# Kernel tuning notes

Measured on AMD Instinct MI355X. Metric: run time of the kernel, lower is better.

## Reference

```python
import jax, jax.numpy as jnp
import numpy as np

D_MODEL = 4096
D_HIDDEN = 32768
BATCH = 2048
K = 128
N_DEAD = 2048


def _ln(x, eps=1e-5):
    # torch .std() is unbiased (ddof=1)
    mu = jnp.mean(x, axis=-1, keepdims=True)
    xc = x - mu
    std = jnp.std(x, axis=-1, keepdims=True, ddof=1)
    return xc / (std + eps), mu, std


def _topk_activation(x, k):
    # topk over last dim, relu values, scatter back into zeros
    vals, idx = jax.lax.top_k(x, k)          # [B, k]
    vals = jax.nn.relu(vals)
    rows = jnp.arange(x.shape[0])[:, None]    # [B, 1]
    return jnp.zeros_like(x).at[rows, idx].set(vals)


def setup_inputs() -> dict:
    key = jax.random.key(0)
    k1, k2 = jax.random.split(key)
    x = jax.random.normal(k1, (BATCH, D_MODEL), dtype=jnp.float32)
    # kaiming-uniform-ish encoder init
    bound = 1.0 / np.sqrt(D_MODEL)
    w_enc = jax.random.uniform(k2, (D_MODEL, D_HIDDEN), dtype=jnp.float32,
                               minval=-bound, maxval=bound)
    w_dec = w_enc.T
    w_dec = w_dec / jnp.linalg.norm(w_dec, axis=0, keepdims=True)
    b_enc = jnp.zeros((D_HIDDEN,), dtype=jnp.float32)
    b_pre = jnp.zeros((D_MODEL,), dtype=jnp.float32)
    # fixed dead-neuron mask with exactly N_DEAD dead latents
    dm = np.zeros((D_HIDDEN,), dtype=bool)
    rng = np.random.default_rng(0)
    dm[rng.choice(D_HIDDEN, size=N_DEAD, replace=False)] = True
    dead_mask = jnp.asarray(dm)
    return {"x": x, "w_enc": w_enc, "w_dec": w_dec, "b_enc": b_enc,
            "b_pre": b_pre, "dead_mask": dead_mask, "num_dead": N_DEAD}


def reference(x, w_enc, w_dec, b_enc, b_pre, dead_mask, num_dead):
    xn, mu, std = _ln(x)
    xc = xn - b_pre
    pre_acts = xc @ w_enc + b_enc                 # [B, d_hidden]
    latents = _topk_activation(pre_acts, K)
    recons = latents @ w_dec + b_pre              # [B, d_model]
    recons = recons * std + mu
    # auxk dead-neuron path (num_dead is a static python int)
    k_aux = min(x.shape[-1] // 2, num_dead)
    auxk_latents = jnp.where(dead_mask[None, :], pre_acts, -jnp.inf)
    auxk_acts = _topk_activation(auxk_latents, k_aux)
    auxk = auxk_acts @ w_dec + b_pre
    auxk = auxk * std + mu
    return recons, auxk, num_dead
```

## Files before the change

kernel.cpp:

```cpp
#include <hip/hip_runtime.h>
#include <math.h>

#define D_MODEL  4096
#define D_HIDDEN 32768
#define BATCH    2048
#define KSEL     128
#define NDEAD    2048
#define TIECAP   256

typedef short s16x8 __attribute__((ext_vector_type(8)));
typedef float f32x4 __attribute__((ext_vector_type(4)));

__device__ __forceinline__ unsigned int fkey(float f) {
    unsigned int u = __float_as_uint(f);
    return (u & 0x80000000u) ? ~u : (u | 0x80000000u);
}
__device__ __forceinline__ unsigned short f2bf(float f) {
    unsigned int u = __float_as_uint(f);
    u += 0x7FFFu + ((u >> 16) & 1u);
    return (unsigned short)(u >> 16);
}
__device__ __forceinline__ float bf2f(unsigned short h) {
    return __uint_as_float(((unsigned int)h) << 16);
}
__device__ __forceinline__ unsigned int key16x2(unsigned int u) {
    const unsigned int s = (u >> 15) & 0x10001u;
    const unsigned int mask = s * 0xFFFFu;
    return (u ^ mask) | (~mask & 0x80008000u);
}
__device__ __forceinline__ float unkey16(unsigned int k) {
    const unsigned int u = (k & 0x8000u) ? (k & 0x7FFFu) : (~k & 0xFFFFu);
    return __uint_as_float(u << 16);
}
__device__ __forceinline__ void async_copy16(void* lds_dst, const void* gsrc) {
    __builtin_amdgcn_global_load_lds(
        (const __attribute__((address_space(1))) unsigned int*)gsrc,
        (__attribute__((address_space(3))) unsigned int*)lds_dst,
        16, 0, 0);
}

__global__ __launch_bounds__(256) void ln_kernel(const float* __restrict__ x,
        double* __restrict__ mu, double* __restrict__ stdv, double* __restrict__ sinv)
{
    const int row = blockIdx.x;
    const int tid = threadIdx.x;
    const float* xr = x + (size_t)row * D_MODEL;
    float xv[16];
#pragma unroll
    for (int i = 0; i < 16; ++i) xv[i] = xr[tid + 256 * i];
    double s = 0.0;
#pragma unroll
    for (int i = 0; i < 16; ++i) s += (double)xv[i];
    __shared__ double red[4];
    __shared__ double sh_mu;
    const int lane = tid & 63, wid = tid >> 6;
#pragma unroll
    for (int off = 32; off > 0; off >>= 1) s += __shfl_down(s, off, 64);
    if (lane == 0) red[wid] = s;
    __syncthreads();
    if (tid == 0) sh_mu = (red[0] + red[1] + red[2] + red[3]) / (double)D_MODEL;
    __syncthreads();
    const double m = sh_mu;
    double s2 = 0.0;
#pragma unroll
    for (int i = 0; i < 16; ++i) { double d = (double)xv[i] - m; s2 += d * d; }
#pragma unroll
    for (int off = 32; off > 0; off >>= 1) s2 += __shfl_down(s2, off, 64);
    __syncthreads();
    if (lane == 0) red[wid] = s2;
    __syncthreads();
    if (tid == 0) {
        double var = (red[0] + red[1] + red[2] + red[3]) / (double)(D_MODEL - 1);
        double sd = sqrt(var);
        mu[row] = m;
        stdv[row] = sd;
        sinv[row] = 1.0 / (sd + 1e-5);
    }
}

__global__ void dead_scan_kernel(const unsigned char* __restrict__ mask8,
                                 int* __restrict__ dead_idx, int* __restrict__ dead_cnt,
                                 const int* __restrict__ num_dead_in, float* __restrict__ out_last)
{
    const int lane = threadIdx.x;
    int c = 0;
    for (int j = lane; j < D_HIDDEN; j += 64) c += (mask8[j] != 0);
#pragma unroll
    for (int off = 32; off > 0; off >>= 1) c += __shfl_down(c, off, 64);
    const int total_u8 = __shfl(c, 0, 64);
    const bool u8mode = (total_u8 == NDEAD);
    const int* mask32 = (const int*)mask8;
    int cnt = 0;
    for (int base = 0; base < D_HIDDEN; base += 64) {
        const int j = base + lane;
        const bool d = u8mode ? (mask8[j] != 0) : (mask32[j] != 0);
        const unsigned long long b = __ballot(d);
        const int pre = __popcll(b & ((1ull << lane) - 1ull));
        if (d && (cnt + pre) < NDEAD) dead_idx[cnt + pre] = j;
        cnt += __popcll(b);
    }
    const int cc = cnt > NDEAD ? NDEAD : cnt;
    if (lane == 0) {
        *dead_cnt = cc;
        *out_last = (float)(*num_dead_in);
    }
    for (int t = cc + lane; t < NDEAD; t += 64) dead_idx[t] = 0;
}

__global__ __launch_bounds__(256) void asplit_kernel(
    const float* __restrict__ x, const double* __restrict__ mu, const double* __restrict__ sinv,
    const float* __restrict__ b_pre, unsigned short* __restrict__ Ahp)
{
    const int row = blockIdx.x, tid = threadIdx.x;
    const double m = mu[row], si = sinv[row];
    const float* xr = x + (size_t)row * D_MODEL;
#pragma unroll
    for (int i = 0; i < 4; ++i) {
        const int j = (i * 256 + tid) * 4;
        const float4 xv = *(const float4*)(xr + j);
        const float4 bp = *(const float4*)(b_pre + j);
        float v[4];
        v[0] = (float)(((double)xv.x - m) * si) - bp.x;
        v[1] = (float)(((double)xv.y - m) * si) - bp.y;
        v[2] = (float)(((double)xv.z - m) * si) - bp.z;
        v[3] = (float)(((double)xv.w - m) * si) - bp.w;
        uint2 hw;
        hw.x = (unsigned)f2bf(v[0]) | ((unsigned)f2bf(v[1]) << 16);
        hw.y = (unsigned)f2bf(v[2]) | ((unsigned)f2bf(v[3]) << 16);
        *(uint2*)(Ahp + (size_t)row * D_MODEL + j) = hw;
    }
}

__global__ __launch_bounds__(256) void bsplit_kernel(
    const float* __restrict__ w_enc, unsigned short* __restrict__ Bhp)
{
    __shared__ float t[32][33];
    const int bk = blockIdx.x * 32;
    const int bn = blockIdx.y * 32;
    const int tid = threadIdx.x;
    const int lr = tid >> 3, lc4 = (tid & 7) * 4;
    const float4 v = *(const float4*)(w_enc + (size_t)(bk + lr) * D_HIDDEN + bn + lc4);
    t[lr][lc4 + 0] = v.x; t[lr][lc4 + 1] = v.y; t[lr][lc4 + 2] = v.z; t[lr][lc4 + 3] = v.w;
    __syncthreads();
    float o[4];
#pragma unroll
    for (int j = 0; j < 4; ++j) o[j] = t[lc4 + j][lr];
    uint2 hw;
    hw.x = (unsigned)f2bf(o[0]) | ((unsigned)f2bf(o[1]) << 16);
    hw.y = (unsigned)f2bf(o[2]) | ((unsigned)f2bf(o[3]) << 16);
    *(uint2*)(Bhp + (size_t)(bn + lr) * D_MODEL + bk + lc4) = hw;
}

__global__ __launch_bounds__(256) void wencT_kernel(
    const float* __restrict__ w_enc, float* __restrict__ wT)
{
    __shared__ float t[32][33];
    const int bk = blockIdx.x * 32;
    const int bn = blockIdx.y * 32;
    const int tid = threadIdx.x;
    const int lr = tid >> 3, lc4 = (tid & 7) * 4;
    const float4 v = *(const float4*)(w_enc + (size_t)(bk + lr) * D_HIDDEN + bn + lc4);
    t[lr][lc4 + 0] = v.x; t[lr][lc4 + 1] = v.y; t[lr][lc4 + 2] = v.z; t[lr][lc4 + 3] = v.w;
    __syncthreads();
    const int j = tid >> 3, i4 = (tid & 7) * 4;
    float4 o;
    o.x = t[i4 + 0][j]; o.y = t[i4 + 1][j]; o.z = t[i4 + 2][j]; o.w = t[i4 + 3][j];
    *(float4*)(wT + (size_t)(bn + j) * D_MODEL + bk + i4) = o;
}

template<int EPI>
__global__ __launch_bounds__(256) void mm_kernel(
    const unsigned short* __restrict__ A, const unsigned short* __restrict__ B,
    const int kdim, const int ntiles_x,
    const float* __restrict__ bias_n,
    const double* __restrict__ muv, const double* __restrict__ stdvv,
    void* __restrict__ outp, const long ostride)
{
    __shared__ unsigned short lds[3 * 2 * 128 * 32];
    const int tid = threadIdx.x;
    const int lane = tid & 63, wid = tid >> 6;
    const int cpx = gridDim.x >> 3;
    const int orig = blockIdx.x;
    const int wg = (orig & 7) * cpx + (orig >> 3);
    const int m0 = (wg % ntiles_x) * 128;
    const int n0 = (wg / ntiles_x) * 128;
    const int wm = (wid >> 1) * 64, wn = (wid & 1) * 64;
    const int fr = lane & 15, kq = lane >> 4;
    const int swr = (fr >> 1) & 3;
    const int qg = (lane & 3) ^ ((lane >> 3) & 3);
    const int qo = (kq ^ swr) * 8;

    f32x4 acc[4][4];
#pragma unroll
    for (int i = 0; i < 4; ++i)
#pragma unroll
        for (int j = 0; j < 4; ++j) acc[i][j] = (f32x4){0.f, 0.f, 0.f, 0.f};

    const unsigned short* srcs[4];
    int d0[4];
#pragma unroll
    for (int j = 0; j < 4; ++j) {
        const int s = wid * 4 + j;
        const int pl = s >> 3, sr = s & 7;
        const int r = sr * 16 + (lane >> 2);
        srcs[j] = (pl ? B : A) + (size_t)((pl ? n0 : m0) + r) * kdim + qg * 8;
        d0[j] = pl * 4096 + sr * 512;
    }

    const int NT = kdim >> 5;
#pragma unroll
    for (int j = 0; j < 4; ++j) async_copy16(lds + 0 * 8192 + d0[j], srcs[j]);
#pragma unroll
    for (int j = 0; j < 4; ++j) async_copy16(lds + 1 * 8192 + d0[j], srcs[j] + 32);

    int cur = 0, nxt = 2;
    for (int t = 0; t < NT; ++t) {
        if (t < NT - 1) {
            asm volatile("s_waitcnt vmcnt(4)" ::: "memory");
        } else {
            asm volatile("s_waitcnt vmcnt(0)" ::: "memory");
        }
        __builtin_amdgcn_s_barrier();
        __builtin_amdgcn_sched_barrier(0);

        if (t + 2 < NT) {
            const int k2 = (t + 2) << 5;
#pragma unroll
            for (int j = 0; j < 4; ++j) async_copy16(lds + nxt * 8192 + d0[j], srcs[j] + k2);
        }

        const unsigned short* la = lds + cur * 8192;
        const unsigned short* lb = la + 4096;
        s16x8 a[4], b[4];
#pragma unroll
        for (int i = 0; i < 4; ++i) {
            a[i] = *(const s16x8*)(la + (wm + i * 16 + fr) * 32 + qo);
            b[i] = *(const s16x8*)(lb + (wn + i * 16 + fr) * 32 + qo);
        }
#pragma unroll
        for (int mi = 0; mi < 4; ++mi)
#pragma unroll
            for (int ni = 0; ni < 4; ++ni)
                acc[mi][ni] = __builtin_amdgcn_mfma_f32_16x16x32_bf16(a[mi], b[ni], acc[mi][ni], 0, 0, 0);

        cur = cur == 2 ? 0 : cur + 1;
        nxt = nxt == 2 ? 0 : nxt + 1;
    }

#pragma unroll
    for (int ni = 0; ni < 4; ++ni) {
        const int col = n0 + wn + ni * 16 + fr;
        const float be = bias_n[col];
#pragma unroll
        for (int mi = 0; mi < 4; ++mi) {
            const int rb = m0 + wm + mi * 16 + kq * 4;
            if (EPI == 0) {
                unsigned short* O = (unsigned short*)outp;
#pragma unroll
                for (int r = 0; r < 4; ++r)
                    O[(size_t)(rb + r) * ostride + col] = f2bf(acc[mi][ni][r] + be);
            } else {
                float* O = (float*)outp;
#pragma unroll
                for (int r = 0; r < 4; ++r) {
                    const int m = rb + r;
                    O[(size_t)m * ostride + col] =
                        (acc[mi][ni][r] + be) * (float)stdvv[m] + (float)muv[m];
                }
            }
        }
    }
}

__global__ __launch_bounds__(256) void topk_sel_kernel(
    const unsigned short* __restrict__ p16,
    int* __restrict__ topk_idx, float* __restrict__ topk_val,
    int* __restrict__ sure_cnt, int* __restrict__ tie_cnt, int* __restrict__ cand_col)
{
    const int row = blockIdx.x;
    const int tid = threadIdx.x;
    const int lane = tid & 63, wid = tid >> 6;
    const unsigned short* pr = p16 + (size_t)row * D_HIDDEN;

    __shared__ int red[4];
    __shared__ int sh_sel, sh_tie;

    uint4 kr[16];
#pragma unroll
    for (int i = 0; i < 16; ++i) {
        uint4 w = *(const uint4*)(pr + (i * 256 + tid) * 8);
        w.x = key16x2(w.x); w.y = key16x2(w.y); w.z = key16x2(w.z); w.w = key16x2(w.w);
        kr[i] = w;
    }
    if (tid == 0) { sh_sel = 0; sh_tie = 0; }

    unsigned int lo = 0, hi = 65535;
    while (lo < hi) {
        const unsigned int mid = (lo + hi) >> 1;
        int c = 0;
#pragma unroll
        for (int i = 0; i < 16; ++i) {
            const unsigned int u[4] = {kr[i].x, kr[i].y, kr[i].z, kr[i].w};
#pragma unroll
            for (int e = 0; e < 4; ++e) {
                c += (int)((u[e] & 0xFFFFu) > mid);
                c += (int)((u[e] >> 16) > mid);
            }
        }
#pragma unroll
        for (int off = 32; off > 0; off >>= 1) c += __shfl_down(c, off, 64);
        if (lane == 0) red[wid] = c;
        __syncthreads();
        const int total = red[0] + red[1] + red[2] + red[3];
        if (total < KSEL) hi = mid; else lo = mid + 1;
        __syncthreads();
    }
    const unsigned int K16 = lo;

    const float vc = unkey16(K16);
    const float DLT = 1.3e-2f;
    const float sureT = vc + 2.f * DLT;
    const float candT = vc - 2.f * DLT;
    const unsigned int sK = fkey(sureT) >> 16;
    const unsigned int cK = fkey(candT) >> 16;

    int* oidx = topk_idx + row * KSEL;
    float* oval = topk_val + row * KSEL;
    int* cc = cand_col + row * TIECAP;
#pragma unroll
    for (int i = 0; i < 16; ++i) {
        const int j0 = (i * 256 + tid) * 8;
        const unsigned int u[4] = {kr[i].x, kr[i].y, kr[i].z, kr[i].w};
#pragma unroll
        for (int e = 0; e < 8; ++e) {
            const unsigned int k = (e & 1) ? (u[e >> 1] >> 16) : (u[e >> 1] & 0xFFFFu);
            if (k < cK) continue;
            const float v = unkey16(k);
            if (k > sK && v > sureT) {
                const int pos = atomicAdd(&sh_sel, 1);
                oidx[pos] = j0 + e;
                oval[pos] = v > 0.f ? v : 0.f;
            } else if (v >= candT) {
                const int t = atomicAdd(&sh_tie, 1);
                if (t < TIECAP) cc[t] = j0 + e;
            }
        }
    }
    __syncthreads();
    if (tid == 0) {
        sure_cnt[row] = sh_sel;
        tie_cnt[row] = sh_tie > TIECAP ? TIECAP : sh_tie;
    }
}

__global__ __launch_bounds__(256) void topk_refine_kernel(
    const int* __restrict__ tie_cnt, const int* __restrict__ cand_col,
    double* __restrict__ cand_val,
    const float* __restrict__ x, const double* __restrict__ mu, const double* __restrict__ sinv,
    const float* __restrict__ b_pre, const float* __restrict__ wT, const float* __restrict__ b_enc)
{
    const int row = blockIdx.x;
    const int tid = threadIdx.x;
    const int lane = tid & 63, wid = tid >> 6;
    const int T = tie_cnt[row];
    const int base = (int)blockIdx.y * 4 + wid;
    if (base >= T) return;
    const double m_ = mu[row], si = sinv[row];
    const float* xr = x + (size_t)row * D_MODEL;
    for (int slot = base; slot < T; slot += 64) {
        const int col = cand_col[row * TIECAP + slot];
        const float* wr = wT + (size_t)col * D_MODEL;
        double s0 = 0.0, s1 = 0.0;
        for (int k = lane * 4; k < D_MODEL; k += 512) {
            {
                const float4 xv = *(const float4*)(xr + k);
                const float4 bp = *(const float4*)(b_pre + k);
                const float4 wv4 = *(const float4*)(wr + k);
                s0 += (((double)xv.x - m_) * si - (double)bp.x) * (double)wv4.x;
                s0 += (((double)xv.y - m_) * si - (double)bp.y) * (double)wv4.y;
                s0 += (((double)xv.z - m_) * si - (double)bp.z) * (double)wv4.z;
                s0 += (((double)xv.w - m_) * si - (double)bp.w) * (double)wv4.w;
            }
            {
                const int k2 = k + 256;
                const float4 xv = *(const float4*)(xr + k2);
                const float4 bp = *(const float4*)(b_pre + k2);
                const float4 wv4 = *(const float4*)(wr + k2);
                s1 += (((double)xv.x - m_) * si - (double)bp.x) * (double)wv4.x;
                s1 += (((double)xv.y - m_) * si - (double)bp.y) * (double)wv4.y;
                s1 += (((double)xv.z - m_) * si - (double)bp.z) * (double)wv4.z;
                s1 += (((double)xv.w - m_) * si - (double)bp.w) * (double)wv4.w;
            }
        }
        double s = s0 + s1;
#pragma unroll
        for (int off = 32; off > 0; off >>= 1) s += __shfl_down(s, off, 64);
        if (lane == 0) cand_val[row * TIECAP + slot] = s + (double)b_enc[col];
    }
}

__global__ __launch_bounds__(256) void topk_fin_kernel(
    const int* __restrict__ sure_cnt, const int* __restrict__ tie_cnt,
    const int* __restrict__ cand_col, const double* __restrict__ cand_val,
    int* __restrict__ topk_idx, float* __restrict__ topk_val)
{
    const int row = blockIdx.x;
    const int tid = threadIdx.x;
    __shared__ double vals[TIECAP];
    __shared__ int cols[TIECAP];
    const int G = sure_cnt[row];
    const int T = tie_cnt[row];
    const int R = KSEL - G;
    if (tid < T) {
        vals[tid] = cand_val[row * TIECAP + tid];
        cols[tid] = cand_col[row * TIECAP + tid];
    }
    __syncthreads();
    int* oidx = topk_idx + row * KSEL;
    float* oval = topk_val + row * KSEL;
    if (tid < T) {
        const double v = vals[tid];
        const int c = cols[tid];
        int rank = 0;
        for (int u = 0; u < T; ++u) {
            const double vu = vals[u];
            rank += (int)((vu > v) || (vu == v && cols[u] < c));
        }
        if (rank < R) {
            oidx[G + rank] = c;
            oval[G + rank] = v > 0.0 ? (float)v : 0.f;
        }
    }
    const int take = R < T ? R : T;
    if (tid >= take && tid < R) {
        oidx[G + tid] = (T > 0) ? cols[0] : 0;
        oval[G + tid] = 0.f;
    }
}

__global__ __launch_bounds__(256) void wdec2bf_kernel(
    const float* __restrict__ w_dec, unsigned short* __restrict__ wd16)
{
    const size_t gid = (size_t)blockIdx.x * 256 + threadIdx.x;
    const size_t base = gid * 8;
    const float4 a = *(const float4*)(w_dec + base);
    const float4 b = *(const float4*)(w_dec + base + 4);
    uint4 o;
    o.x = (unsigned)f2bf(a.x) | ((unsigned)f2bf(a.y) << 16);
    o.y = (unsigned)f2bf(a.z) | ((unsigned)f2bf(a.w) << 16);
    o.z = (unsigned)f2bf(b.x) | ((unsigned)f2bf(b.y) << 16);
    o.w = (unsigned)f2bf(b.z) | ((unsigned)f2bf(b.w) << 16);
    *(uint4*)(wd16 + base) = o;
}

__global__ __launch_bounds__(256) void decode_kernel(
    const int* __restrict__ topk_idx, const float* __restrict__ topk_val,
    const unsigned short* __restrict__ wd16, const float* __restrict__ b_pre,
    const double* __restrict__ mu, const double* __restrict__ stdv,
    float* __restrict__ out0)
{
    const int row = blockIdx.x;
    const int tid = threadIdx.x;
    __shared__ int sidx[KSEL];
    __shared__ float sval[KSEL];
    if (tid < KSEL) {
        sidx[tid] = topk_idx[row * KSEL + tid];
        sval[tid] = topk_val[row * KSEL + tid];
    }
    __syncthreads();
    float acc[16];
#pragma unroll
    for (int i = 0; i < 16; ++i) acc[i] = 0.f;
    const int dbase = tid * 16;
    for (int k = 0; k < KSEL; ++k) {
        const float v = sval[k];
        if (v == 0.f) continue;
        const uint4* wr = (const uint4*)(wd16 + (size_t)sidx[k] * D_MODEL + dbase);
        const uint4 w0 = wr[0], w1 = wr[1];
        const unsigned int u[8] = {w0.x, w0.y, w0.z, w0.w, w1.x, w1.y, w1.z, w1.w};
#pragma unroll
        for (int i = 0; i < 8; ++i) {
            acc[2 * i]     += v * __uint_as_float(u[i] << 16);
            acc[2 * i + 1] += v * __uint_as_float(u[i] & 0xFFFF0000u);
        }
    }
    const float st = (float)stdv[row];
    const float mm = (float)mu[row];
    float* o = out0 + (size_t)row * D_MODEL + dbase;
#pragma unroll
    for (int i = 0; i < 16; ++i) {
        o[i] = (acc[i] + b_pre[dbase + i]) * st + mm;
    }
}

__global__ __launch_bounds__(256) void auxg_kernel(
    const unsigned short* __restrict__ p16, const int* __restrict__ dead_idx,
    const int* __restrict__ dead_cnt, unsigned short* __restrict__ Ahd)
{
    const int r = blockIdx.x;
    const int tid = threadIdx.x;
    const int dc = *dead_cnt;
#pragma unroll
    for (int i = 0; i < 8; ++i) {
        const int c = i * 256 + tid;
        unsigned short v = 0;
        if (c < dc) {
            const unsigned short u = p16[(size_t)r * D_HIDDEN + dead_idx[c]];
            v = (u & 0x8000u) ? (unsigned short)0 : u;
        }
        Ahd[(size_t)r * NDEAD + c] = v;
    }
}

__global__ __launch_bounds__(256) void auxb_kernel(
    const float* __restrict__ w_dec, const int* __restrict__ dead_idx,
    unsigned short* __restrict__ Bhd)
{
    __shared__ float t[32][33];
    const int k0 = blockIdx.x * 32;
    const int n0 = blockIdx.y * 32;
    const int tid = threadIdx.x;
    const int i = tid >> 3, j4 = (tid & 7) * 4;
    const int srow = dead_idx[k0 + i];
    const float4 v = *(const float4*)(w_dec + (size_t)srow * D_MODEL + n0 + j4);
    t[i][j4 + 0] = v.x; t[i][j4 + 1] = v.y; t[i][j4 + 2] = v.z; t[i][j4 + 3] = v.w;
    __syncthreads();
    const int j = tid >> 3, i4 = (tid & 7) * 4;
    uint2 hw;
    hw.x = (unsigned)f2bf(t[i4 + 0][j]) | ((unsigned)f2bf(t[i4 + 1][j]) << 16);
    hw.y = (unsigned)f2bf(t[i4 + 2][j]) | ((unsigned)f2bf(t[i4 + 3][j]) << 16);
    *(uint2*)(Bhd + (size_t)(n0 + j) * NDEAD + k0 + i4) = hw;
}

extern "C" void kernel_launch(void* const* d_in, const int* in_sizes, int n_in,
                              void* d_out, int out_size, void* d_ws, size_t ws_size,
                              hipStream_t stream)
{
    (void)in_sizes; (void)n_in; (void)out_size; (void)ws_size;
    const float* x      = (const float*)d_in[0];
    const float* w_enc  = (const float*)d_in[1];
    const float* w_dec  = (const float*)d_in[2];
    const float* b_enc  = (const float*)d_in[3];
    const float* b_pre  = (const float*)d_in[4];
    const unsigned char* dead_mask = (const unsigned char*)d_in[5];
    const int* num_dead = (const int*)d_in[6];
    float* out = (float*)d_out;

    char* base = (char*)d_ws;
    char* w = base;
    auto alloc = [&](size_t bytes) -> char* {
        char* p = w;
        w += (bytes + 255) & ~(size_t)255;
        return p;
    };
    unsigned short* p16 = (unsigned short*)alloc((size_t)BATCH * D_HIDDEN * 2);
    double* mu       = (double*)alloc((size_t)BATCH * 8);
    double* stdv     = (double*)alloc((size_t)BATCH * 8);
    double* sinv     = (double*)alloc((size_t)BATCH * 8);
    int* topk_idx    = (int*)alloc((size_t)BATCH * KSEL * 4);
    float* topk_val  = (float*)alloc((size_t)BATCH * KSEL * 4);
    int* dead_idx    = (int*)alloc((size_t)NDEAD * 4);
    int* dead_cnt    = (int*)alloc(256);
    int* sure_cnt    = (int*)alloc((size_t)BATCH * 4);
    int* tie_cnt     = (int*)alloc((size_t)BATCH * 4);
    int* cand_col    = (int*)alloc((size_t)BATCH * TIECAP * 4);
    double* cand_val = (double*)alloc((size_t)BATCH * TIECAP * 8);
    unsigned short* Ahp = (unsigned short*)alloc((size_t)BATCH * D_MODEL * 2);
    char* region     = alloc((size_t)D_HIDDEN * D_MODEL * 4);

    unsigned short* Bhp = (unsigned short*)region;
    float* wT   = (float*)region;
    unsigned short* wd16 = (unsigned short*)region;
    unsigned short* Bhd  = (unsigned short*)(region + (size_t)D_HIDDEN * D_MODEL * 2);
    unsigned short* Ahd  = Ahp;

    float* out0 = out;
    float* out1 = out + (size_t)BATCH * D_MODEL;
    float* out_last = out + (size_t)2 * BATCH * D_MODEL;

    ln_kernel<<<BATCH, 256, 0, stream>>>(x, mu, stdv, sinv);
    dead_scan_kernel<<<1, 64, 0, stream>>>(dead_mask, dead_idx, dead_cnt, num_dead, out_last);
    asplit_kernel<<<BATCH, 256, 0, stream>>>(x, mu, sinv, b_pre, Ahp);
    bsplit_kernel<<<dim3(D_MODEL / 32, D_HIDDEN / 32), 256, 0, stream>>>(w_enc, Bhp);
    mm_kernel<0><<<(BATCH / 128) * (D_HIDDEN / 128), 256, 0, stream>>>(
        Ahp, Bhp, D_MODEL, BATCH / 128, b_enc, nullptr, nullptr, p16, (long)D_HIDDEN);
    wencT_kernel<<<dim3(D_MODEL / 32, D_HIDDEN / 32), 256, 0, stream>>>(w_enc, wT);
    topk_sel_kernel<<<BATCH, 256, 0, stream>>>(p16, topk_idx, topk_val, sure_cnt, tie_cnt, cand_col);
    topk_refine_kernel<<<dim3(BATCH, 16), 256, 0, stream>>>(
        tie_cnt, cand_col, cand_val, x, mu, sinv, b_pre, wT, b_enc);
    topk_fin_kernel<<<BATCH, 256, 0, stream>>>(
        sure_cnt, tie_cnt, cand_col, cand_val, topk_idx, topk_val);
    auxg_kernel<<<BATCH, 256, 0, stream>>>(p16, dead_idx, dead_cnt, Ahd);
    auxb_kernel<<<dim3(NDEAD / 32, D_MODEL / 32), 256, 0, stream>>>(w_dec, dead_idx, Bhd);
    wdec2bf_kernel<<<(int)(((size_t)D_HIDDEN * D_MODEL) / (256 * 8)), 256, 0, stream>>>(w_dec, wd16);
    decode_kernel<<<BATCH, 256, 0, stream>>>(topk_idx, topk_val, wd16, b_pre, mu, stdv, out0);
    mm_kernel<1><<<(BATCH / 128) * (D_MODEL / 128), 256, 0, stream>>>(
        Ahd, Bhd, NDEAD, BATCH / 128, b_pre, mu, stdv, out1, (long)D_MODEL);
}
```

Measured before the change: 2.405 ms.

## Use 256x256-tile, 512-thread bf16 MFMA kernel for the encoder GEMM

Adds a new GEMM kernel with 256x256 output tiles, 8 waves per block, double-buffered async LDS loads over a BK=64 K-step, and uses it for the large encoder matmul instead of the 128x128 kernel. The bigger tile raises arithmetic intensity and cuts global/L2 traffic per FLOP for the 2048x32768x4096 product. In exchange it uses 128 accumulator vectors per thread and 128KB of LDS, which lowers occupancy and may cause register pressure, and it drops from triple to double buffering.

After: 2.294 ms. 1.05x faster.

```diff
diff --git a/kernel.cpp b/kernel.cpp
--- a/kernel.cpp
+++ b/kernel.cpp
@@ -166,6 +166,114 @@
     float4 o;
     o.x = t[i4 + 0][j]; o.y = t[i4 + 1][j]; o.z = t[i4 + 2][j]; o.w = t[i4 + 3][j];
     *(float4*)(wT + (size_t)(bn + j) * D_MODEL + bk + i4) = o;
+}
+
+template<int EPI>
+__global__ __launch_bounds__(512) void mm256_kernel(
+    const unsigned short* __restrict__ A, const unsigned short* __restrict__ B,
+    const int kdim, const int ntiles_x,
+    const float* __restrict__ bias_n,
+    const double* __restrict__ muv, const double* __restrict__ stdvv,
+    void* __restrict__ outp, const long ostride)
+{
+    __shared__ unsigned short lds[2 * 4 * 8192];
+    const int tid = threadIdx.x;
+    const int lane = tid & 63, wid = tid >> 6;
+    const int cpx = gridDim.x >> 3;
+    const int orig = blockIdx.x;
+    const int wg = (orig & 7) * cpx + (orig >> 3);
+    const int m0 = (wg % ntiles_x) * 256;
+    const int n0 = (wg / ntiles_x) * 256;
+    const int wm = (wid >> 2) * 128;
+    const int wn = (wid & 3) * 64;
+    const int fr = lane & 15, kq = lane >> 4;
+    const int swr = (fr >> 1) & 3;
+    const int qg = (lane & 3) ^ ((lane >> 3) & 3);
+    const int qo = (kq ^ swr) * 8;
+
+    f32x4 acc[8][4];
+#pragma unroll
+    for (int i = 0; i < 8; ++i)
+#pragma unroll
+        for (int j = 0; j < 4; ++j) acc[i][j] = (f32x4){0.f, 0.f, 0.f, 0.f};
+
+    const unsigned short* srcs[8];
+    int d0[8];
+#pragma unroll
+    for (int j = 0; j < 8; ++j) {
+        const int s = wid * 8 + j;
+        const int sp = s >> 4, sr = s & 15;
+        const unsigned short* gp = (sp < 2) ? A : B;
+        const int t0 = (sp < 2) ? m0 : n0;
+        const int row = sr * 16 + (lane >> 2);
+        srcs[j] = gp + (size_t)(t0 + row) * kdim + (sp & 1) * 32 + qg * 8;
+        d0[j] = sp * 8192 + sr * 512;
+    }
+
+    const int NT = kdim >> 6;
+#pragma unroll
+    for (int j = 0; j < 8; ++j) async_copy16(lds + d0[j], srcs[j]);
+
+    for (int t = 0; t < NT; ++t) {
+        const int cur = t & 1;
+        if (t + 1 < NT) {
+            const int k1 = (t + 1) << 6;
+#pragma unroll
+            for (int j = 0; j < 8; ++j)
+                async_copy16(lds + (cur ^ 1) * 32768 + d0[j], srcs[j] + k1);
+            asm volatile("s_waitcnt vmcnt(8)" ::: "memory");
+        } else {
+            asm volatile("s_waitcnt vmcnt(0)" ::: "memory");
+        }
+        __builtin_amdgcn_s_barrier();
+        __builtin_amdgcn_sched_barrier(0);
+
+        const unsigned short* bb = lds + cur * 32768;
+#pragma unroll
+        for (int kk = 0; kk < 2; ++kk) {
+            s16x8 a[8], b[4];
+#pragma unroll
+            for (int mi = 0; mi < 8; ++mi)
+                a[mi] = *(const s16x8*)(bb + kk * 8192 + (wm + mi * 16 + fr) * 32 + qo);
+#pragma unroll
+            for (int ni = 0; ni < 4; ++ni)
+                b[ni] = *(const s16x8*)(bb + (2 + kk) * 8192 + (wn + ni * 16 + fr) * 32 + qo);
+            __builtin_amdgcn_s_setprio(1);
+#pragma unroll
+            for (int mi = 0; mi < 8; ++mi)
+#pragma unroll
+                for (int ni = 0; ni < 4; ++ni)
+                    acc[mi][ni] = __builtin_amdgcn_mfma_f32_16x16x32_bf16(a[mi], b[ni], acc[mi][ni], 0, 0, 0);
+            __builtin_amdgcn_s_setprio(0);
+        }
+        __builtin_amdgcn_sched_barrier(0);
+        __builtin_amdgcn_s_barrier();
+        __builtin_amdgcn_sched_barrier(0);
+    }
+
+#pragma unroll
+    for (int ni = 0; ni < 4; ++ni) {
+        const int col = n0 + wn + ni * 16 + fr;
+        const float be = bias_n[col];
+#pragma unroll
+        for (int mi = 0; mi < 8; ++mi) {
+            const int rb = m0 + wm + mi * 16 + kq * 4;
+            if (EPI == 0) {
+                unsigned short* O = (unsigned short*)outp;
+#pragma unroll
+                for (int r = 0; r < 4; ++r)
+                    O[(size_t)(rb + r) * ostride + col] = f2bf(acc[mi][ni][r] + be);
+            } else {
+                float* O = (float*)outp;
+#pragma unroll
+                for (int r = 0; r < 4; ++r) {
+                    const int m = rb + r;
+                    O[(size_t)m * ostride + col] =
+                        (acc[mi][ni][r] + be) * (float)stdvv[m] + (float)muv[m];
+                }
+            }
+        }
+    }
 }
 
 template<int EPI>
@@ -582,8 +690,8 @@
     dead_scan_kernel<<<1, 64, 0, stream>>>(dead_mask, dead_idx, dead_cnt, num_dead, out_last);
     asplit_kernel<<<BATCH, 256, 0, stream>>>(x, mu, sinv, b_pre, Ahp);
     bsplit_kernel<<<dim3(D_MODEL / 32, D_HIDDEN / 32), 256, 0, stream>>>(w_enc, Bhp);
-    mm_kernel<0><<<(BATCH / 128) * (D_HIDDEN / 128), 256, 0, stream>>>(
-        Ahp, Bhp, D_MODEL, BATCH / 128, b_enc, nullptr, nullptr, p16, (long)D_HIDDEN);
+    mm256_kernel<0><<<(BATCH / 256) * (D_HIDDEN / 256), 512, 0, stream>>>(
+        Ahp, Bhp, D_MODEL, BATCH / 256, b_enc, nullptr, nullptr, p16, (long)D_HIDDEN);
     wencT_kernel<<<dim3(D_MODEL / 32, D_HIDDEN / 32), 256, 0, stream>>>(w_enc, wT);
     topk_sel_kernel<<<BATCH, 256, 0, stream>>>(p16, topk_idx, topk_val, sure_cnt, tie_cnt, cand_col);
     topk_refine_kernel<<<dim3(BATCH, 16), 256, 0, stream>>>(
```
